# Kernel tuning notes

Hardware: AMD Instinct MI355X
Metric: run time of the kernel (lower is better)

Reference implementation:

```python
import jax, jax.numpy as jnp
import numpy as np
from jax import lax

DIM = 128; D_STATE = 16; D_CONV = 4; D_INNER = 256; DT_RANK = 8
N_HEADS = 4; SPARSE_RATIO = 0.5; LN_EPS = 1e-5


def rmsnorm(x, w):
    return x * lax.rsqrt(jnp.mean(x * x, axis=-1, keepdims=True) + 1e-5) * w


def layernorm(x, w, b):
    mu = jnp.mean(x, axis=-1, keepdims=True)
    var = jnp.mean((x - mu) ** 2, axis=-1, keepdims=True)
    return (x - mu) * lax.rsqrt(var + LN_EPS) * w + b


def mamba(x, in_proj_w, conv1d_w, conv1d_b, x_proj_w, dt_proj_w, dt_proj_b, A_log, Dp, out_proj_w):
    # x: (N, L, d_model) -> selective scan over L
    N, L, _ = x.shape
    xz = x @ in_proj_w.T                              # (N, L, 2*d_inner)
    xc, zg = jnp.split(xz, 2, axis=-1)
    xc = xc.transpose(0, 2, 1)                        # (N, d_inner, L)
    xc = lax.conv_general_dilated(xc, conv1d_w, (1,), [(D_CONV - 1, 0)],
                                  feature_group_count=D_INNER,
                                  dimension_numbers=('NCH', 'OIH', 'NCH'))
    xc = jax.nn.silu(xc + conv1d_b[None, :, None]).transpose(0, 2, 1)  # (N, L, d_inner)
    x_dbl = xc @ x_proj_w.T
    dt, Bm, Cm = jnp.split(x_dbl, [DT_RANK, DT_RANK + D_STATE], axis=-1)
    dt = jax.nn.softplus(dt @ dt_proj_w.T + dt_proj_b)  # (N, L, d_inner)
    A = -jnp.exp(A_log)                                  # (d_inner, d_state)

    def step(h, ts):
        dt_t, B_t, C_t, u_t = ts                         # (N,di),(N,ds),(N,ds),(N,di)
        h = h * jnp.exp(dt_t[:, :, None] * A) + (dt_t * u_t)[:, :, None] * B_t[:, None, :]
        y = jnp.einsum('nds,ns->nd', h, C_t)
        return h, y

    h0 = jnp.zeros((N, D_INNER, D_STATE), x.dtype)
    ts = (dt.transpose(1, 0, 2), Bm.transpose(1, 0, 2), Cm.transpose(1, 0, 2), xc.transpose(1, 0, 2))
    _, ys = lax.scan(step, h0, ts)
    y = ys.transpose(1, 0, 2) + xc * Dp
    y = y * jax.nn.silu(zg)
    return y @ out_proj_w.T


def setup_inputs() -> dict:
    key = jax.random.key(0)
    ks = jax.random.split(key, 16)
    s = 0.02
    B, T, C, H, W = 8, 8, 128, 32, 32
    rn = lambda k, shp: (jax.random.normal(k, shp, jnp.float32) * s)
    return {
        'x_in': jax.random.normal(ks[0], (B, T, C, H, W), jnp.float32),
        'norm1_w': jnp.ones((DIM,), jnp.float32),
        'in_proj_w': rn(ks[1], (2 * D_INNER, DIM)),
        'conv1d_w': rn(ks[2], (D_INNER, 1, D_CONV)),
        'conv1d_b': jnp.zeros((D_INNER,), jnp.float32),
        'x_proj_w': rn(ks[3], (DT_RANK + 2 * D_STATE, D_INNER)),
        'dt_proj_w': rn(ks[4], (D_INNER, DT_RANK)),
        'dt_proj_b': jax.random.uniform(ks[5], (D_INNER,), jnp.float32, -0.1, 0.1),
        'A_log': jnp.log(jnp.broadcast_to(jnp.arange(1, D_STATE + 1, dtype=jnp.float32), (D_INNER, D_STATE))),
        'D': jnp.ones((D_INNER,), jnp.float32),
        'out_proj_w': rn(ks[6], (DIM, D_INNER)),
        'r1_w': rn(ks[7], (DIM // 4, DIM, 3, 3)),
        'r1_b': jnp.zeros((DIM // 4,), jnp.float32),
        'r2_w': rn(ks[8], (1, DIM // 4, 1, 1)),
        'r2_b': jnp.zeros((1,), jnp.float32),
        'attn_in_w': rn(ks[9], (3 * DIM, DIM)),
        'attn_in_b': jnp.zeros((3 * DIM,), jnp.float32),
        'attn_out_w': rn(ks[10], (DIM, DIM)),
        'attn_out_b': jnp.zeros((DIM,), jnp.float32),
        'ln_w': jnp.ones((DIM,), jnp.float32),
        'ln_b': jnp.zeros((DIM,), jnp.float32),
        'current_epoch': 20,
    }


def reference(x_in, norm1_w, in_proj_w, conv1d_w, conv1d_b, x_proj_w, dt_proj_w, dt_proj_b,
              A_log, D, out_proj_w, r1_w, r1_b, r2_w, r2_b, attn_in_w, attn_in_b,
              attn_out_w, attn_out_b, ln_w, ln_b, current_epoch):
    B, T, C, H, W = x_in.shape
    N = H * W
    # annealed sparse ratio: current_epoch (static int) >= anneal_end -> target ratio
    ratio = SPARSE_RATIO if current_epoch >= 10 else (0.0 if current_epoch < 5 else SPARSE_RATIO * (current_epoch - 5) / 5.0)
    K = max(1, int(N * (1.0 - ratio)))
    # ---- learnable router scores (eval mode: no noise) ----
    xm = jnp.mean(x_in, axis=1)                       # (B,C,H,W)
    h1 = lax.conv_general_dilated(xm, r1_w, (1, 1), [(1, 1), (1, 1)],
                                  dimension_numbers=('NCHW', 'OIHW', 'NCHW')) + r1_b[None, :, None, None]
    h1 = jnp.where(h1 >= 0, h1, 0.01 * h1)            # LeakyReLU(0.01)
    sc = lax.conv_general_dilated(h1, r2_w, (1, 1), [(0, 0), (0, 0)],
                                  dimension_numbers=('NCHW', 'OIHW', 'NCHW')) + r2_b[None, :, None, None]
    scores = jax.nn.sigmoid(sc).reshape(B, N)
    _, idx = lax.top_k(scores, K)
    idx = jnp.sort(idx, axis=1)                        # (B,K)
    bi = jnp.arange(B)[:, None]
    x_flat = x_in.transpose(0, 3, 4, 1, 2).reshape(B, N, T, C)
    x_g = x_flat[bi, idx]                              # (B,K,T,C)
    s_g = scores[bi, idx]
    x_sp = x_g * (s_g / (lax.stop_gradient(s_g) + 1e-6))[:, :, None, None]  # STE scaling
    # ---- time mixing: Mamba on each kept spatial token ----
    z = rmsnorm(x_sp.reshape(B * K, T, C), norm1_w)
    z = mamba(z, in_proj_w, conv1d_w, conv1d_b, x_proj_w, dt_proj_w, dt_proj_b, A_log, D, out_proj_w)
    # ---- spatial self-attention over K tokens per time step ----
    zs = z.reshape(B, K, T, C).transpose(0, 2, 1, 3).reshape(B * T, K, C)
    qkv = zs @ attn_in_w.T + attn_in_b
    q, k, v = jnp.split(qkv, 3, axis=-1)
    dh = C // N_HEADS
    heads = lambda t: t.reshape(B * T, K, N_HEADS, dh).transpose(0, 2, 1, 3)
    q, k, v = heads(q), heads(k), heads(v)
    attn = jax.nn.softmax(jnp.einsum('bhqd,bhkd->bhqk', q, k) / np.sqrt(dh).astype(np.float32), axis=-1)
    o = jnp.einsum('bhqk,bhkd->bhqd', attn, v).transpose(0, 2, 1, 3).reshape(B * T, K, C)
    o = o @ attn_out_w.T + attn_out_b
    z_out = layernorm(zs + o, ln_w, ln_b)
    # ---- densify (scatter back) & residual ----
    upd = z_out.reshape(B, T, K, C).transpose(0, 2, 1, 3)  # (B,K,T,C)
    dense = jnp.zeros((B, N, T, C), x_in.dtype).at[bi, idx].set(upd)
    return x_in + dense.reshape(B, H, W, T, C).transpose(0, 3, 4, 1, 2)
```

## Files before the change

### kernel.cpp

```cpp
#include <hip/hip_runtime.h>
#include <hip/hip_bf16.h>

typedef __hip_bfloat16 bf16;
typedef __attribute__((ext_vector_type(8))) short short8;
typedef __attribute__((ext_vector_type(4))) float f32x4;

#define KK 512

__device__ float g_xm[1048576];
__device__ float g_h1[262144];
__device__ float g_scal[4096];
__device__ int   g_idx[4096];
__device__ float g_xg[4194304];
__device__ float g_zs[4194304];
__device__ float g_qkv[12582912];
__device__ float g_o[4194304];
__device__ float g_xz[16777216];
__device__ float g_xc[8388608];
__device__ float g_xdbl[1310720];
__device__ float g_y[8388608];
__device__ float g_wint[65536];
__device__ float g_wot[16384];
__device__ ushort g_wqkvh[49152];
__device__ ushort g_wouth[32768];
__device__ float g_A[4096];
__device__ float g_zo[4194304];

__device__ __forceinline__ float b2f(bf16 v) { return __bfloat162float(v); }

__device__ __forceinline__ ushort f2bu(float f) {
    union { float f; unsigned u; } v; v.f = f;
    unsigned r = v.u + 0x7fffu + ((v.u >> 16) & 1u);
    return (ushort)(r >> 16);
}

union U8 { short8 v; ushort u[8]; };

__global__ void k_mean(const float* __restrict__ x) {
    int id = blockIdx.x * 256 + threadIdx.x;
    int n = id & 1023;
    int c = (id >> 10) & 127;
    int b = id >> 17;
    float s = 0.f;
#pragma unroll
    for (int t = 0; t < 8; ++t)
        s += x[(((b * 8 + t) * 128 + c) << 10) + n];
    g_xm[id] = s * 0.125f;
}

__global__ __launch_bounds__(1024) void k_rconv1(const float* __restrict__ w) {
    __shared__ float xs[4][1024];
    int blk = blockIdx.x;
    int icc = blk & 31, b = blk >> 5;
    int ic0 = icc * 4;
    int tid = threadIdx.x;
    int x = tid & 31, y = tid >> 5;
#pragma unroll
    for (int i = 0; i < 4; ++i)
        xs[i][tid] = g_xm[b * 131072 + (ic0 + i) * 1024 + tid];
    __syncthreads();

    float xv[4][9];
#pragma unroll
    for (int i = 0; i < 4; ++i)
#pragma unroll
        for (int ky = 0; ky < 3; ++ky)
#pragma unroll
            for (int kx = 0; kx < 3; ++kx) {
                int yy = y + ky - 1, xx = x + kx - 1;
                bool ok = (yy >= 0) && (yy < 32) && (xx >= 0) && (xx < 32);
                xv[i][ky * 3 + kx] = ok ? xs[i][yy * 32 + xx] : 0.f;
            }

    float* rp = g_xz;
#pragma unroll 2
    for (int oc = 0; oc < 32; ++oc) {
        const float* wr = w + (oc * 128 + ic0) * 9;
        float acc = 0.f;
#pragma unroll
        for (int i = 0; i < 4; ++i)
#pragma unroll
            for (int t = 0; t < 9; ++t)
                acc += xv[i][t] * wr[i * 9 + t];
        rp[((size_t)(icc * 8 + b) * 32 + oc) * 1024 + tid] = acc;
    }
}

__global__ void k_rconv2(const float* __restrict__ bias) {
    int id = blockIdx.x * 256 + threadIdx.x;
    int oc = (id >> 10) & 31;
    const float* rp = g_xz;
    float acc = bias[oc];
#pragma unroll 8
    for (int icc = 0; icc < 32; ++icc)
        acc += rp[(size_t)icc * 262144 + id];
    g_h1[id] = acc >= 0.f ? acc : 0.01f * acc;
}

__global__ __launch_bounds__(1024) void k_topk(const float* __restrict__ r2w,
                                               const float* __restrict__ r2b) {
    __shared__ float sc[1024];
    __shared__ int flg[1024];
    int b = blockIdx.x;
    int n = threadIdx.x;
    float a = r2b[0];
#pragma unroll
    for (int ic = 0; ic < 32; ++ic)
        a += g_h1[b * 32768 + ic * 1024 + n] * r2w[ic];
    float s = 1.f / (1.f + expf(-a));
    sc[n] = s;
    __syncthreads();
    int rank = 0;
    for (int j = 0; j < 1024; ++j) {
        float v = sc[j];
        rank += (v > s) || (v == s && j < n);
    }
    int sel = rank < KK ? 1 : 0;
    flg[n] = sel;
    __syncthreads();
    for (int d = 1; d < 1024; d <<= 1) {
        int add = (n >= d) ? flg[n - d] : 0;
        __syncthreads();
        flg[n] += add;
        __syncthreads();
    }
    if (sel) {
        int pos = (flg[n] - 1) & 511;
        g_idx[b * KK + pos] = n;
        g_scal[b * KK + pos] = s / (s + 1e-6f);
    }
}

__global__ __launch_bounds__(256) void k_gather(const float* __restrict__ x) {
    __shared__ float lds[16][1024];
    int blk = blockIdx.x;
    int cchunk = blk & 7;
    int t = (blk >> 3) & 7;
    int b = blk >> 6;
    int c0 = cchunk * 16;
    int tid = threadIdx.x;
    const float* src = x + ((size_t)(b * 8 + t) * 128 + c0) * 1024;
#pragma unroll
    for (int r = 0; r < 64; ++r) {
        int e = tid + r * 256;
        lds[e >> 10][e & 1023] = src[e];
    }
    __syncthreads();
#pragma unroll
    for (int half = 0; half < 2; ++half) {
        int k = tid + half * 256;
        int n = g_idx[b * KK + k] & 1023;
        float scl = fminf(fmaxf(g_scal[b * KK + k], 0.f), 1.f);
        float* dst = g_xg + ((size_t)(b * 512 + k) * 8 + t) * 128 + c0;
#pragma unroll
        for (int cc = 0; cc < 16; ++cc)
            dst[cc] = lds[cc][n] * scl;
    }
}

__global__ void k_wt(const float* __restrict__ w_in, const float* __restrict__ w_out,
                     const float* __restrict__ w_ao, const float* __restrict__ A_log,
                     const float* __restrict__ w_qkv) {
    int e = blockIdx.x * 256 + threadIdx.x;
    if (e < 65536) { int j = e >> 7; int c = e & 127; g_wint[c * 512 + j] = w_in[e]; }
    if (e < 32768) { g_wouth[e] = f2bu(w_out[e]); }
    if (e < 16384) { int i = e >> 7; int c = e & 127; g_wot[c * 128 + i] = w_ao[e]; }
    if (e < 49152) { g_wqkvh[e] = f2bu(w_qkv[e]); }
    if (e < 4096)  { g_A[e] = -expf(A_log[e]);
                     g_scal[e] = 1.0f; g_idx[e] = e & 511; }
}

template<int KTOT, int NTOT, int JW, int NSPLIT, int MODE>
__global__ __launch_bounds__(512) void k_proj(const float* __restrict__ bias,
                                              const float* __restrict__ conv_w,
                                              const float* __restrict__ conv_b) {
    __shared__ float Xs[64 * 129];
    const float* A  = (MODE == 0) ? g_xg : g_o;
    const float* Bt = (MODE == 0) ? g_wint : g_wot;
    float* Cc       = g_xz;
    int blk = blockIdx.x;
    int ncol0 = (blk % NSPLIT) * (NTOT / NSPLIT);
    int row0 = (blk / NSPLIT) * 64;
    int tid = threadIdx.x;
    int lane = tid & 63;
    int j0 = __builtin_amdgcn_readfirstlane(ncol0 + (tid >> 6) * JW);
    float acc[JW];
#pragma unroll
    for (int j = 0; j < JW; ++j) acc[j] = 0.f;
    float ss = 0.f;

    for (int kc = 0; kc < KTOT; kc += 128) {
        __syncthreads();
#pragma unroll
        for (int i = 0; i < 4; ++i) {
            int e4 = tid + i * 512;
            int r = e4 >> 5, c4 = e4 & 31;
            float4 v = *(const float4*)&A[(size_t)(row0 + r) * KTOT + kc + c4 * 4];
            float* xp = &Xs[r * 129 + c4 * 4];
            xp[0] = v.x; xp[1] = v.y; xp[2] = v.z; xp[3] = v.w;
        }
        __syncthreads();
        const float* xr = &Xs[lane * 129];
        const float* wbase = Bt + (size_t)kc * NTOT + j0;
#pragma unroll 2
        for (int k4 = 0; k4 < 32; ++k4) {
            float a0 = xr[k4 * 4 + 0], a1 = xr[k4 * 4 + 1];
            float a2 = xr[k4 * 4 + 2], a3 = xr[k4 * 4 + 3];
            if (MODE == 0) {
                float4 nw = *(const float4*)(bias + kc + k4 * 4);
                ss += a0 * a0 + a1 * a1 + a2 * a2 + a3 * a3;
                a0 *= nw.x; a1 *= nw.y; a2 *= nw.z; a3 *= nw.w;
            }
            const float* wb = wbase + (size_t)k4 * 4 * NTOT;
#pragma unroll
            for (int jj = 0; jj < JW / 4; ++jj) {
                float4 w0 = *(const float4*)(wb + jj * 4);
                float4 w1 = *(const float4*)(wb + NTOT + jj * 4);
                float4 w2 = *(const float4*)(wb + 2 * NTOT + jj * 4);
                float4 w3 = *(const float4*)(wb + 3 * NTOT + jj * 4);
                float s0 = acc[jj*4+0], s1 = acc[jj*4+1], s2 = acc[jj*4+2], s3 = acc[jj*4+3];
                s0 += a0 * w0.x; s1 += a0 * w0.y; s2 += a0 * w0.z; s3 += a0 * w0.w;
                s0 += a1 * w1.x; s1 += a1 * w1.y; s2 += a1 * w1.z; s3 += a1 * w1.w;
                s0 += a2 * w2.x; s1 += a2 * w2.y; s2 += a2 * w2.z; s3 += a2 * w2.w;
                s0 += a3 * w3.x; s1 += a3 * w3.y; s2 += a3 * w3.z; s3 += a3 * w3.w;
                acc[jj*4+0] = s0; acc[jj*4+1] = s1; acc[jj*4+2] = s2; acc[jj*4+3] = s3;
            }
        }
    }

    if (MODE == 0) {
        float rstd = rsqrtf(ss * (1.f / 128.f) + 1e-5f);
#pragma unroll
        for (int j = 0; j < JW; ++j) acc[j] *= rstd;
    }

    int row = row0 + lane;
    if (MODE == 0 && j0 < 256) {
        int t = lane & 7;
        float* dst = g_xc + (size_t)row * 256 + j0;
#pragma unroll
        for (int jj = 0; jj < JW / 4; ++jj) {
            float4 vv;
            float* vp = (float*)&vv;
#pragma unroll
            for (int q = 0; q < 4; ++q) {
                int j = jj * 4 + q;
                float x3 = acc[j];
                float x2 = __shfl_up(x3, 1, 64); if (t < 1) x2 = 0.f;
                float x1 = __shfl_up(x3, 2, 64); if (t < 2) x1 = 0.f;
                float x0 = __shfl_up(x3, 3, 64); if (t < 3) x0 = 0.f;
                float4 w4 = *(const float4*)(conv_w + (j0 + j) * 4);
                float v = x0 * w4.x + x1 * w4.y + x2 * w4.z + x3 * w4.w + conv_b[j0 + j];
                vp[q] = v * __builtin_amdgcn_rcpf(1.f + __expf(-v));
            }
            *(float4*)(dst + jj * 4) = vv;
        }
    } else if (MODE == 3) {
        __shared__ float red1[8][64];
        __shared__ float red2[8][64];
        int w = tid >> 6;
        __syncthreads();
#pragma unroll
        for (int i = 0; i < 4; ++i) {
            int e4 = tid + i * 512;
            int r = e4 >> 5, c4 = e4 & 31;
            float4 v = *(const float4*)&g_zs[(size_t)(row0 + r) * 128 + c4 * 4];
            float* xp = &Xs[r * 129 + c4 * 4];
            xp[0] = v.x; xp[1] = v.y; xp[2] = v.z; xp[3] = v.w;
        }
        __syncthreads();
        float s1 = 0.f, s2 = 0.f;
#pragma unroll
        for (int j = 0; j < JW; ++j) {
            acc[j] += bias[j0 + j] + Xs[lane * 129 + j0 + j];
            s1 += acc[j]; s2 += acc[j] * acc[j];
        }
        red1[w][lane] = s1; red2[w][lane] = s2;
        __syncthreads();
        float S1 = 0.f, S2 = 0.f;
#pragma unroll
        for (int ww = 0; ww < 8; ++ww) { S1 += red1[ww][lane]; S2 += red2[ww][lane]; }
        float mu = S1 * (1.f / 128.f);
        float var = S2 * (1.f / 128.f) - mu * mu;
        float rstd2 = rsqrtf(fmaxf(var, 0.f) + 1e-5f);
        int bt = row >> 9, ktok = row & 511;
        float* zb = g_zo + (size_t)(bt * 128 + j0) * 512 + ktok;
#pragma unroll
        for (int j = 0; j < JW; ++j)
            zb[(size_t)j * 512] = (acc[j] - mu) * rstd2 * conv_w[j0 + j] + conv_b[j0 + j];
    } else {
        float* dst = Cc + (size_t)row * NTOT + j0;
#pragma unroll
        for (int jj = 0; jj < JW / 4; ++jj)
            *(float4*)(dst + jj * 4) =
                make_float4(acc[jj*4], acc[jj*4+1], acc[jj*4+2], acc[jj*4+3]);
    }
}

__global__ __launch_bounds__(256) void k_outm() {
    __shared__ ushort As[8][64][40];
    __shared__ ushort Bs[128][40];
    int row0 = blockIdx.x * 64;
    int tid = threadIdx.x;
    int w = tid >> 6, lane = tid & 63;
    int c = lane & 15, g = lane >> 4;

    {
        int r = tid >> 2, ksb = tid & 3;
#pragma unroll
        for (int kb2 = 0; kb2 < 2; ++kb2) {
            int kb = ksb + kb2 * 4;
            const float* src = g_y + (size_t)(row0 + r) * 256 + kb * 32;
#pragma unroll
            for (int i = 0; i < 4; ++i) {
                float4 a = *(const float4*)(src + i * 8);
                float4 b = *(const float4*)(src + i * 8 + 4);
                U8 t;
                t.u[0] = f2bu(a.x); t.u[1] = f2bu(a.y); t.u[2] = f2bu(a.z); t.u[3] = f2bu(a.w);
                t.u[4] = f2bu(b.x); t.u[5] = f2bu(b.y); t.u[6] = f2bu(b.z); t.u[7] = f2bu(b.w);
                *(short8*)&As[kb][r][i * 8] = t.v;
            }
        }
    }

    f32x4 acc[8];
    f32x4 zero = {0.f, 0.f, 0.f, 0.f};
#pragma unroll
    for (int nt = 0; nt < 8; ++nt) acc[nt] = zero;

    for (int ks = 0; ks < 8; ++ks) {
        __syncthreads();
#pragma unroll
        for (int i = 0; i < 2; ++i) {
            int e = tid + i * 256;
            int n = e >> 2, q = e & 3;
            *(short8*)&Bs[n][q * 8] =
                *(const short8*)&g_wouth[n * 256 + ks * 32 + q * 8];
        }
        __syncthreads();
        short8 af = *(const short8*)&As[ks][w * 16 + c][g * 8];
#pragma unroll
        for (int nt = 0; nt < 8; ++nt) {
            short8 bf8 = *(const short8*)&Bs[nt * 16 + c][g * 8];
            acc[nt] = __builtin_amdgcn_mfma_f32_16x16x32_bf16(af, bf8, acc[nt], 0, 0, 0);
        }
    }

#pragma unroll
    for (int r = 0; r < 4; ++r) {
        int row = row0 + w * 16 + g * 4 + r;
        int bb = row >> 12, kk2 = (row >> 3) & 511, t = row & 7;
        float* dst = g_zs + ((size_t)((bb * 8 + t) * 512 + kk2)) * 128 + c;
#pragma unroll
        for (int nt = 0; nt < 8; ++nt)
            dst[nt * 16] = acc[nt][r];
    }
}

__global__ __launch_bounds__(256) void k_qkvm(const float* __restrict__ bias) {
    __shared__ ushort As[4][64][40];
    __shared__ ushort Bs[384][40];
    int row0 = blockIdx.x * 64;
    int tid = threadIdx.x;
    int w = tid >> 6, lane = tid & 63;
    int c = lane & 15, g = lane >> 4;

    {
        int r = tid >> 2, ksb = tid & 3;
        const float* src = g_zs + (size_t)(row0 + r) * 128 + ksb * 32;
#pragma unroll
        for (int i = 0; i < 4; ++i) {
            float4 a = *(const float4*)(src + i * 8);
            float4 b = *(const float4*)(src + i * 8 + 4);
            U8 t;
            t.u[0] = f2bu(a.x); t.u[1] = f2bu(a.y); t.u[2] = f2bu(a.z); t.u[3] = f2bu(a.w);
            t.u[4] = f2bu(b.x); t.u[5] = f2bu(b.y); t.u[6] = f2bu(b.z); t.u[7] = f2bu(b.w);
            *(short8*)&As[ksb][r][i * 8] = t.v;
        }
    }

    f32x4 acc[24];
    f32x4 zero = {0.f, 0.f, 0.f, 0.f};
#pragma unroll
    for (int nt = 0; nt < 24; ++nt) acc[nt] = zero;

    for (int ks = 0; ks < 4; ++ks) {
        __syncthreads();
#pragma unroll
        for (int i = 0; i < 6; ++i) {
            int e = tid + i * 256;
            int n = e >> 2, q = e & 3;
            *(short8*)&Bs[n][q * 8] =
                *(const short8*)&g_wqkvh[n * 128 + ks * 32 + q * 8];
        }
        __syncthreads();
        short8 af = *(const short8*)&As[ks][w * 16 + c][g * 8];
#pragma unroll
        for (int nt = 0; nt < 24; ++nt) {
            short8 bf8 = *(const short8*)&Bs[nt * 16 + c][g * 8];
            acc[nt] = __builtin_amdgcn_mfma_f32_16x16x32_bf16(af, bf8, acc[nt], 0, 0, 0);
        }
    }

#pragma unroll
    for (int nt = 0; nt < 24; ++nt) {
        float bv = bias[nt * 16 + c];
#pragma unroll
        for (int r = 0; r < 4; ++r) {
            int tok = row0 + w * 16 + g * 4 + r;
            g_qkv[(size_t)tok * 384 + nt * 16 + c] = acc[nt][r] + bv;
        }
    }
}

__global__ __launch_bounds__(512, 2) void k_xproj(const float* __restrict__ w_xp) {
    __shared__ float Xs[64][66];
    int row0 = blockIdx.x * 64;
    int tid = threadIdx.x;
    int lane = tid & 63;
    int j0 = __builtin_amdgcn_readfirstlane((tid >> 6) * 5);
    float acc0 = 0.f, acc1 = 0.f, acc2 = 0.f, acc3 = 0.f, acc4 = 0.f;

    for (int kc = 0; kc < 4; ++kc) {
        __syncthreads();
#pragma unroll
        for (int i = 0; i < 2; ++i) {
            int e = tid + i * 512;
            int r = e >> 4, k4 = e & 15;
            *(float4*)&Xs[r][k4 * 4] =
                *(const float4*)&g_xc[(size_t)(row0 + r) * 256 + kc * 64 + k4 * 4];
        }
        __syncthreads();
#pragma unroll
        for (int k4 = 0; k4 < 16; ++k4) {
            float4 x4 = *(const float4*)&Xs[lane][k4 * 4];
            const float* wb = w_xp + kc * 64 + k4 * 4;
            float4 w0 = *(const float4*)(wb + (j0 + 0) * 256);
            float4 w1 = *(const float4*)(wb + (j0 + 1) * 256);
            float4 w2 = *(const float4*)(wb + (j0 + 2) * 256);
            float4 w3 = *(const float4*)(wb + (j0 + 3) * 256);
            float4 w4 = *(const float4*)(wb + (j0 + 4) * 256);
            acc0 += x4.x * w0.x + x4.y * w0.y + x4.z * w0.z + x4.w * w0.w;
            acc1 += x4.x * w1.x + x4.y * w1.y + x4.z * w1.z + x4.w * w1.w;
            acc2 += x4.x * w2.x + x4.y * w2.y + x4.z * w2.z + x4.w * w2.w;
            acc3 += x4.x * w3.x + x4.y * w3.y + x4.z * w3.z + x4.w * w3.w;
            acc4 += x4.x * w4.x + x4.y * w4.y + x4.z * w4.z + x4.w * w4.w;
        }
    }
    float* dst = g_xdbl + (size_t)(row0 + lane) * 40 + j0;
    dst[0] = acc0; dst[1] = acc1; dst[2] = acc2; dst[3] = acc3; dst[4] = acc4;
}

__global__ __launch_bounds__(256, 2) void k_scan2(const float* __restrict__ w_dt,
                        const float* __restrict__ b_dt, const float* __restrict__ Dp) {
    int tok = blockIdx.x;
    int d = threadIdx.x;
    const float* xzr = g_xz + (size_t)tok * 4096;
    const float* xcr = g_xc + (size_t)tok * 2048;
    const float* xd0 = g_xdbl + (size_t)tok * 320;
    float* yr = g_y + (size_t)tok * 2048;

    float4 wdt0 = *(const float4*)(w_dt + d * 8);
    float4 wdt1 = *(const float4*)(w_dt + d * 8 + 4);
    float bdt = b_dt[d];
    float Dd = Dp[d];
    float Av[16], h[16];
#pragma unroll
    for (int s = 0; s < 4; ++s) {
        float4 a4 = *(const float4*)(g_A + d * 16 + s * 4);
        Av[4*s] = a4.x; Av[4*s+1] = a4.y; Av[4*s+2] = a4.z; Av[4*s+3] = a4.w;
    }
#pragma unroll
    for (int s = 0; s < 16; ++s) h[s] = 0.f;

#pragma unroll
    for (int t = 0; t < 8; ++t) {
        const float* xd = xd0 + t * 40;
        float dtv = bdt
            + xd[0] * wdt0.x + xd[1] * wdt0.y + xd[2] * wdt0.z + xd[3] * wdt0.w
            + xd[4] * wdt1.x + xd[5] * wdt1.y + xd[6] * wdt1.z + xd[7] * wdt1.w;
        dtv = dtv > 20.f ? dtv : logf(1.f + expf(dtv));
        float u = xcr[t * 256 + d];
        float db = dtv * u;
        float y = 0.f;
#pragma unroll
        for (int s = 0; s < 16; ++s) {
            h[s] = h[s] * __expf(dtv * Av[s]) + db * xd[8 + s];
            y += h[s] * xd[24 + s];
        }
        y += u * Dd;
        float zg = xzr[t * 512 + 256 + d];
        y *= zg * __builtin_amdgcn_rcpf(1.f + __expf(-zg));
        yr[t * 256 + d] = y;
    }
}

#define ATTN_LDS 74240
__global__ __launch_bounds__(256, 2) void k_attn3() {
    extern __shared__ char smem[];
    ushort* Kl = (ushort*)smem;
    ushort* Vt = (ushort*)(smem + 40960);
    ushort* Pl = (ushort*)smem;
    __shared__ float statsM[4][32];
    __shared__ float statsS[4][32];

    int blk = blockIdx.x;
    int qt = blk & 3, h = (blk >> 2) & 3, bt = blk >> 4;
    int q0 = qt * 32;
    int tid = threadIdx.x;
    int w = tid >> 6, lane = tid & 63;
    int c = lane & 15, g = lane >> 4;
    const float* QKV = g_qkv + (size_t)bt * 512 * 384;
    const float rs = 0.17677669529663687f;

    short8 qf[2];
#pragma unroll
    for (int i = 0; i < 2; ++i) {
        const float* qp = QKV + (size_t)(q0 + i * 16 + c) * 384 + h * 32 + g * 8;
        float4 a = *(const float4*)qp;
        float4 b = *(const float4*)(qp + 4);
        U8 t;
        t.u[0] = f2bu(a.x * rs); t.u[1] = f2bu(a.y * rs);
        t.u[2] = f2bu(a.z * rs); t.u[3] = f2bu(a.w * rs);
        t.u[4] = f2bu(b.x * rs); t.u[5] = f2bu(b.y * rs);
        t.u[6] = f2bu(b.z * rs); t.u[7] = f2bu(b.w * rs);
        qf[i] = t.v;
    }

#pragma unroll
    for (int r = 0; r < 8; ++r) {
        int tok = r * 64 + (tid >> 2);
        int dblk = (tid & 3) * 8;
        const float* kp = QKV + (size_t)tok * 384 + 128 + h * 32 + dblk;
        float4 ka = *(const float4*)kp,       kb4 = *(const float4*)(kp + 4);
        float4 va = *(const float4*)(kp+128), vb4 = *(const float4*)(kp + 132);
        U8 t;
        t.u[0] = f2bu(ka.x); t.u[1] = f2bu(ka.y); t.u[2] = f2bu(ka.z); t.u[3] = f2bu(ka.w);
        t.u[4] = f2bu(kb4.x); t.u[5] = f2bu(kb4.y); t.u[6] = f2bu(kb4.z); t.u[7] = f2bu(kb4.w);
        *(short8*)&Kl[tok * 40 + dblk] = t.v;
        Vt[(dblk + 0) * 520 + tok] = f2bu(va.x);
        Vt[(dblk + 1) * 520 + tok] = f2bu(va.y);
        Vt[(dblk + 2) * 520 + tok] = f2bu(va.z);
        Vt[(dblk + 3) * 520 + tok] = f2bu(va.w);
        Vt[(dblk + 4) * 520 + tok] = f2bu(vb4.x);
        Vt[(dblk + 5) * 520 + tok] = f2bu(vb4.y);
        Vt[(dblk + 6) * 520 + tok] = f2bu(vb4.z);
        Vt[(dblk + 7) * 520 + tok] = f2bu(vb4.w);
    }
    __syncthreads();

    int kbase = w * 128;
    f32x4 S[2][8];
    f32x4 zero = {0.f, 0.f, 0.f, 0.f};
#pragma unroll
    for (int ks = 0; ks < 8; ++ks) {
        short8 kf = *(const short8*)&Kl[(kbase + ks * 16 + c) * 40 + g * 8];
        S[0][ks] = __builtin_amdgcn_mfma_f32_16x16x32_bf16(qf[0], kf, zero, 0, 0, 0);
        S[1][ks] = __builtin_amdgcn_mfma_f32_16x16x32_bf16(qf[1], kf, zero, 0, 0, 0);
    }

    float pmax[2][4];
#pragma unroll
    for (int i = 0; i < 2; ++i)
#pragma unroll
        for (int r = 0; r < 4; ++r) {
            float m = S[i][0][r];
#pragma unroll
            for (int ks = 1; ks < 8; ++ks) m = fmaxf(m, S[i][ks][r]);
            pmax[i][r] = m;
        }
#pragma unroll
    for (int msk = 1; msk <= 8; msk <<= 1)
#pragma unroll
        for (int i = 0; i < 2; ++i)
#pragma unroll
            for (int r = 0; r < 4; ++r)
                pmax[i][r] = fmaxf(pmax[i][r], __shfl_xor(pmax[i][r], msk, 64));
    if (c == 0) {
#pragma unroll
        for (int i = 0; i < 2; ++i)
#pragma unroll
            for (int r = 0; r < 4; ++r)
                statsM[w][i * 16 + g * 4 + r] = pmax[i][r];
    }
    __syncthreads();

    float psum[2][4];
#pragma unroll
    for (int i = 0; i < 2; ++i)
#pragma unroll
        for (int r = 0; r < 4; ++r) {
            int q = i * 16 + g * 4 + r;
            float m = fmaxf(fmaxf(statsM[0][q], statsM[1][q]),
                            fmaxf(statsM[2][q], statsM[3][q]));
            float ps = 0.f;
#pragma unroll
            for (int ks = 0; ks < 8; ++ks) {
                float p = __expf(S[i][ks][r] - m);
                ps += p;
                Pl[q * 520 + kbase + ks * 16 + c] = f2bu(p);
            }
            psum[i][r] = ps;
        }
#pragma unroll
    for (int msk = 1; msk <= 8; msk <<= 1)
#pragma unroll
        for (int i = 0; i < 2; ++i)
#pragma unroll
            for (int r = 0; r < 4; ++r)
                psum[i][r] += __shfl_xor(psum[i][r], msk, 64);
    if (c == 0) {
#pragma unroll
        for (int i = 0; i < 2; ++i)
#pragma unroll
            for (int r = 0; r < 4; ++r)
                statsS[w][i * 16 + g * 4 + r] = psum[i][r];
    }
    __syncthreads();

    f32x4 o[2][2];
    o[0][0] = zero; o[0][1] = zero; o[1][0] = zero; o[1][1] = zero;
#pragma unroll
    for (int kst = 0; kst < 4; ++kst) {
        int k0 = kbase + kst * 32;
        short8 pa0 = *(const short8*)&Pl[(c) * 520 + k0 + g * 8];
        short8 pa1 = *(const short8*)&Pl[(16 + c) * 520 + k0 + g * 8];
        short8 vb0 = *(const short8*)&Vt[(c) * 520 + k0 + g * 8];
        short8 vb1 = *(const short8*)&Vt[(16 + c) * 520 + k0 + g * 8];
        o[0][0] = __builtin_amdgcn_mfma_f32_16x16x32_bf16(pa0, vb0, o[0][0], 0, 0, 0);
        o[0][1] = __builtin_amdgcn_mfma_f32_16x16x32_bf16(pa0, vb1, o[0][1], 0, 0, 0);
        o[1][0] = __builtin_amdgcn_mfma_f32_16x16x32_bf16(pa1, vb0, o[1][0], 0, 0, 0);
        o[1][1] = __builtin_amdgcn_mfma_f32_16x16x32_bf16(pa1, vb1, o[1][1], 0, 0, 0);
    }
    __syncthreads();

    float* Op = (float*)smem;
#pragma unroll
    for (int i = 0; i < 2; ++i)
#pragma unroll
        for (int jd = 0; jd < 2; ++jd)
#pragma unroll
            for (int r = 0; r < 4; ++r)
                Op[(w * 32 + i * 16 + g * 4 + r) * 33 + jd * 16 + c] = o[i][jd][r];
    __syncthreads();

    int q = tid >> 3;
    int d0 = (tid & 7) * 4;
    float lrow = statsS[0][q] + statsS[1][q] + statsS[2][q] + statsS[3][q];
    float inv = 1.f / lrow;
    float* orow = g_o + ((size_t)(bt * 512) + q0 + q) * 128 + h * 32 + d0;
#pragma unroll
    for (int dd = 0; dd < 4; ++dd) {
        float s = Op[(0 * 32 + q) * 33 + d0 + dd] + Op[(1 * 32 + q) * 33 + d0 + dd]
                + Op[(2 * 32 + q) * 33 + d0 + dd] + Op[(3 * 32 + q) * 33 + d0 + dd];
        orow[dd] = s * inv;
    }
}

__global__ __launch_bounds__(256) void k_fin2(const float* __restrict__ x_in,
                                              float* __restrict__ out) {
    __shared__ float dense[1024];
    int R = blockIdx.x;
    int bt = R >> 7;
    int b = bt >> 3;
    int tid = threadIdx.x;
#pragma unroll
    for (int i = 0; i < 4; ++i) dense[tid + i * 256] = 0.f;
    __syncthreads();
#pragma unroll
    for (int hh = 0; hh < 2; ++hh) {
        int k = tid + hh * 256;
        int n = g_idx[b * KK + k] & 1023;
        dense[n] = g_zo[(size_t)R * 512 + k];
    }
    __syncthreads();
    const float4* xr = (const float4*)(x_in + (size_t)R * 1024);
    const float4* dn = (const float4*)dense;
    float4* orr = (float4*)(out + (size_t)R * 1024);
    float4 xv = xr[tid], dv = dn[tid];
    float4 ov;
    ov.x = xv.x + dv.x; ov.y = xv.y + dv.y; ov.z = xv.z + dv.z; ov.w = xv.w + dv.w;
    orr[tid] = ov;
}

extern "C" void kernel_launch(void* const* d_in, const int* in_sizes, int n_in,
                              void* d_out, int out_size, void* d_ws, size_t ws_size,
                              hipStream_t stream) {
    const float* x_in      = (const float*)d_in[0];
    const float* norm1_w   = (const float*)d_in[1];
    const float* in_proj_w = (const float*)d_in[2];
    const float* conv1d_w  = (const float*)d_in[3];
    const float* conv1d_b  = (const float*)d_in[4];
    const float* x_proj_w  = (const float*)d_in[5];
    const float* dt_proj_w = (const float*)d_in[6];
    const float* dt_proj_b = (const float*)d_in[7];
    const float* A_log     = (const float*)d_in[8];
    const float* Dp        = (const float*)d_in[9];
    const float* out_proj_w= (const float*)d_in[10];
    const float* r1_w      = (const float*)d_in[11];
    const float* r1_b      = (const float*)d_in[12];
    const float* r2_w      = (const float*)d_in[13];
    const float* r2_b      = (const float*)d_in[14];
    const float* attn_in_w = (const float*)d_in[15];
    const float* attn_in_b = (const float*)d_in[16];
    const float* attn_out_w= (const float*)d_in[17];
    const float* attn_out_b= (const float*)d_in[18];
    const float* ln_w      = (const float*)d_in[19];
    const float* ln_b      = (const float*)d_in[20];

    float* out = (float*)d_out;

    static bool attr_set = false;
    if (!attr_set) {
        hipFuncSetAttribute(reinterpret_cast<const void*>(k_attn3),
                            hipFuncAttributeMaxDynamicSharedMemorySize, ATTN_LDS);
        attr_set = true;
    }

    k_wt<<<256, 256, 0, stream>>>(in_proj_w, out_proj_w, attn_out_w, A_log, attn_in_w);
    k_mean<<<4096, 256, 0, stream>>>(x_in);
    k_rconv1<<<256, 1024, 0, stream>>>(r1_w);
    k_rconv2<<<1024, 256, 0, stream>>>(r1_b);
    k_topk<<<8, 1024, 0, stream>>>(r2_w, r2_b);
    k_gather<<<512, 256, 0, stream>>>(x_in);
    k_proj<128, 512, 32, 2, 0><<<1024, 512, 0, stream>>>(norm1_w, conv1d_w, conv1d_b);
    k_xproj<<<512, 512, 0, stream>>>(x_proj_w);
    k_scan2<<<4096, 256, 0, stream>>>(dt_proj_w, dt_proj_b, Dp);
    k_outm<<<512, 256, 0, stream>>>();
    k_qkvm<<<512, 256, 0, stream>>>(attn_in_b);
    k_attn3<<<1024, 256, ATTN_LDS, stream>>>();
    k_proj<128, 128, 16, 1, 3><<<512, 512, 0, stream>>>(attn_out_b, ln_w, ln_b);
    k_fin2<<<8192, 256, 0, stream>>>(x_in, out);
}
```

Baseline: 470.1 us.

## Use split-bf16 MFMA for in-projection and split depthwise conv into own kernel

The fp32 FMA in-projection GEMM is replaced by a matrix-core kernel that splits activations and weights into high and low bf16 parts and runs three MFMAs per tile, keeping near-fp32 accuracy. RMSNorm weights are folded into the preprocessed weights, and the row scale is applied after the matmul. The causal conv plus SiLU, previously fused into the GEMM epilogue, now runs as a separate kernel that reads g_xz, which adds a global round trip and an extra launch. The out-proj/LayerNorm path is moved unchanged into a dedicated kernel.

```diff
diff --git a/kernel.cpp b/kernel.cpp
--- a/kernel.cpp
+++ b/kernel.cpp
@@ -19,7 +19,8 @@
 __device__ float g_xc[8388608];
 __device__ float g_xdbl[1310720];
 __device__ float g_y[8388608];
-__device__ float g_wint[65536];
+__device__ ushort g_winth[65536];
+__device__ ushort g_wintl[65536];
 __device__ float g_wot[16384];
 __device__ ushort g_wqkvh[49152];
 __device__ ushort g_wouth[32768];
@@ -32,6 +33,9 @@
     union { float f; unsigned u; } v; v.f = f;
     unsigned r = v.u + 0x7fffu + ((v.u >> 16) & 1u);
     return (ushort)(r >> 16);
+}
+__device__ __forceinline__ float bu2f(ushort u) {
+    union { unsigned u; float f; } v; v.u = ((unsigned)u) << 16; return v.f;
 }
 
 union U8 { short8 v; ushort u[8]; };
@@ -160,9 +164,15 @@
 
 __global__ void k_wt(const float* __restrict__ w_in, const float* __restrict__ w_out,
                      const float* __restrict__ w_ao, const float* __restrict__ A_log,
-                     const float* __restrict__ w_qkv) {
+                     const float* __restrict__ w_qkv, const float* __restrict__ nw) {
     int e = blockIdx.x * 256 + threadIdx.x;
-    if (e < 65536) { int j = e >> 7; int c = e & 127; g_wint[c * 512 + j] = w_in[e]; }
+    if (e < 65536) {
+        int k = e & 127;
+        float wf = w_in[e] * nw[k];
+        ushort h = f2bu(wf);
+        g_winth[e] = h;
+        g_wintl[e] = f2bu(wf - bu2f(h));
+    }
     if (e < 32768) { g_wouth[e] = f2bu(w_out[e]); }
     if (e < 16384) { int i = e >> 7; int c = e & 127; g_wot[c * 128 + i] = w_ao[e]; }
     if (e < 49152) { g_wqkvh[e] = f2bu(w_qkv[e]); }
@@ -170,130 +180,101 @@
                      g_scal[e] = 1.0f; g_idx[e] = e & 511; }
 }
 
-template<int KTOT, int NTOT, int JW, int NSPLIT, int MODE>
-__global__ __launch_bounds__(512) void k_proj(const float* __restrict__ bias,
-                                              const float* __restrict__ conv_w,
+__global__ __launch_bounds__(256) void k_inm() {
+    __shared__ ushort Ah[4][64][40];
+    __shared__ ushort Al[4][64][40];
+    __shared__ ushort Bh[128][40];
+    __shared__ ushort Bl[128][40];
+    __shared__ float sR[64];
+    int blk = blockIdx.x;
+    int ncol0 = (blk & 3) * 128;
+    int row0 = (blk >> 2) * 64;
+    int tid = threadIdx.x;
+    int w = tid >> 6, lane = tid & 63;
+    int c = lane & 15, g = lane >> 4;
+
+    {
+        int r = tid >> 2, ksb = tid & 3;
+        const float* src = g_xg + (size_t)(row0 + r) * 128 + ksb * 32;
+        float ss = 0.f;
+#pragma unroll
+        for (int i = 0; i < 4; ++i) {
+            float4 a = *(const float4*)(src + i * 8);
+            float4 b = *(const float4*)(src + i * 8 + 4);
+            float xv[8] = {a.x, a.y, a.z, a.w, b.x, b.y, b.z, b.w};
+            U8 th, tl;
+#pragma unroll
+            for (int q = 0; q < 8; ++q) {
+                float x = xv[q];
+                ss += x * x;
+                ushort h = f2bu(x);
+                th.u[q] = h;
+                tl.u[q] = f2bu(x - bu2f(h));
+            }
+            *(short8*)&Ah[ksb][r][i * 8] = th.v;
+            *(short8*)&Al[ksb][r][i * 8] = tl.v;
+        }
+        ss += __shfl_xor(ss, 1, 64);
+        ss += __shfl_xor(ss, 2, 64);
+        if ((tid & 3) == 0) sR[r] = rsqrtf(ss * (1.f / 128.f) + 1e-5f);
+    }
+
+    f32x4 acc[8];
+    f32x4 zero = {0.f, 0.f, 0.f, 0.f};
+#pragma unroll
+    for (int nt = 0; nt < 8; ++nt) acc[nt] = zero;
+
+    for (int ks = 0; ks < 4; ++ks) {
+        __syncthreads();
+#pragma unroll
+        for (int i = 0; i < 2; ++i) {
+            int e = tid + i * 256;
+            int n = e >> 2, q = e & 3;
+            *(short8*)&Bh[n][q * 8] =
+                *(const short8*)&g_winth[(ncol0 + n) * 128 + ks * 32 + q * 8];
+            *(short8*)&Bl[n][q * 8] =
+                *(const short8*)&g_wintl[(ncol0 + n) * 128 + ks * 32 + q * 8];
+        }
+        __syncthreads();
+        short8 ah = *(const short8*)&Ah[ks][w * 16 + c][g * 8];
+        short8 al = *(const short8*)&Al[ks][w * 16 + c][g * 8];
+#pragma unroll
+        for (int nt = 0; nt < 8; ++nt) {
+            short8 bh = *(const short8*)&Bh[nt * 16 + c][g * 8];
+            short8 bl = *(const short8*)&Bl[nt * 16 + c][g * 8];
+            acc[nt] = __builtin_amdgcn_mfma_f32_16x16x32_bf16(ah, bh, acc[nt], 0, 0, 0);
+            acc[nt] = __builtin_amdgcn_mfma_f32_16x16x32_bf16(ah, bl, acc[nt], 0, 0, 0);
+            acc[nt] = __builtin_amdgcn_mfma_f32_16x16x32_bf16(al, bh, acc[nt], 0, 0, 0);
+        }
+    }
+
+#pragma unroll
+    for (int r = 0; r < 4; ++r) {
+        int rowl = w * 16 + g * 4 + r;
+        float rs_ = sR[rowl];
+        float* dst = g_xz + (size_t)(row0 + rowl) * 512 + ncol0 + c;
+#pragma unroll
+        for (int nt = 0; nt < 8; ++nt)
+            dst[nt * 16] = acc[nt][r] * rs_;
+    }
+}
+
+__global__ __launch_bounds__(256) void k_conv(const float* __restrict__ conv_w,
                                               const float* __restrict__ conv_b) {
-    __shared__ float Xs[64 * 129];
-    const float* A  = (MODE == 0) ? g_xg : g_o;
-    const float* Bt = (MODE == 0) ? g_wint : g_wot;
-    float* Cc       = g_xz;
-    int blk = blockIdx.x;
-    int ncol0 = (blk % NSPLIT) * (NTOT / NSPLIT);
-    int row0 = (blk / NSPLIT) * 64;
-    int tid = threadIdx.x;
-    int lane = tid & 63;
-    int j0 = __builtin_amdgcn_readfirstlane(ncol0 + (tid >> 6) * JW);
-    float acc[JW];
-#pragma unroll
-    for (int j = 0; j < JW; ++j) acc[j] = 0.f;
-    float ss = 0.f;
-
-    for (int kc = 0; kc < KTOT; kc += 128) {
-        __syncthreads();
-#pragma unroll
-        for (int i = 0; i < 4; ++i) {
-            int e4 = tid + i * 512;
-            int r = e4 >> 5, c4 = e4 & 31;
-            float4 v = *(const float4*)&A[(size_t)(row0 + r) * KTOT + kc + c4 * 4];
-            float* xp = &Xs[r * 129 + c4 * 4];
-            xp[0] = v.x; xp[1] = v.y; xp[2] = v.z; xp[3] = v.w;
-        }
-        __syncthreads();
-        const float* xr = &Xs[lane * 129];
-        const float* wbase = Bt + (size_t)kc * NTOT + j0;
-#pragma unroll 2
-        for (int k4 = 0; k4 < 32; ++k4) {
-            float a0 = xr[k4 * 4 + 0], a1 = xr[k4 * 4 + 1];
-            float a2 = xr[k4 * 4 + 2], a3 = xr[k4 * 4 + 3];
-            if (MODE == 0) {
-                float4 nw = *(const float4*)(bias + kc + k4 * 4);
-                ss += a0 * a0 + a1 * a1 + a2 * a2 + a3 * a3;
-                a0 *= nw.x; a1 *= nw.y; a2 *= nw.z; a3 *= nw.w;
-            }
-            const float* wb = wbase + (size_t)k4 * 4 * NTOT;
-#pragma unroll
-            for (int jj = 0; jj < JW / 4; ++jj) {
-                float4 w0 = *(const float4*)(wb + jj * 4);
-                float4 w1 = *(const float4*)(wb + NTOT + jj * 4);
-                float4 w2 = *(const float4*)(wb + 2 * NTOT + jj * 4);
-                float4 w3 = *(const float4*)(wb + 3 * NTOT + jj * 4);
-                float s0 = acc[jj*4+0], s1 = acc[jj*4+1], s2 = acc[jj*4+2], s3 = acc[jj*4+3];
-                s0 += a0 * w0.x; s1 += a0 * w0.y; s2 += a0 * w0.z; s3 += a0 * w0.w;
-                s0 += a1 * w1.x; s1 += a1 * w1.y; s2 += a1 * w1.z; s3 += a1 * w1.w;
-                s0 += a2 * w2.x; s1 += a2 * w2.y; s2 += a2 * w2.z; s3 += a2 * w2.w;
-                s0 += a3 * w3.x; s1 += a3 * w3.y; s2 += a3 * w3.z; s3 += a3 * w3.w;
-                acc[jj*4+0] = s0; acc[jj*4+1] = s1; acc[jj*4+2] = s2; acc[jj*4+3] = s3;
-            }
-        }
-    }
-
-    if (MODE == 0) {
-        float rstd = rsqrtf(ss * (1.f / 128.f) + 1e-5f);
-#pragma unroll
-        for (int j = 0; j < JW; ++j) acc[j] *= rstd;
-    }
-
-    int row = row0 + lane;
-    if (MODE == 0 && j0 < 256) {
-        int t = lane & 7;
-        float* dst = g_xc + (size_t)row * 256 + j0;
-#pragma unroll
-        for (int jj = 0; jj < JW / 4; ++jj) {
-            float4 vv;
-            float* vp = (float*)&vv;
-#pragma unroll
-            for (int q = 0; q < 4; ++q) {
-                int j = jj * 4 + q;
-                float x3 = acc[j];
-                float x2 = __shfl_up(x3, 1, 64); if (t < 1) x2 = 0.f;
-                float x1 = __shfl_up(x3, 2, 64); if (t < 2) x1 = 0.f;
-                float x0 = __shfl_up(x3, 3, 64); if (t < 3) x0 = 0.f;
-                float4 w4 = *(const float4*)(conv_w + (j0 + j) * 4);
-                float v = x0 * w4.x + x1 * w4.y + x2 * w4.z + x3 * w4.w + conv_b[j0 + j];
-                vp[q] = v * __builtin_amdgcn_rcpf(1.f + __expf(-v));
-            }
-            *(float4*)(dst + jj * 4) = vv;
-        }
-    } else if (MODE == 3) {
-        __shared__ float red1[8][64];
-        __shared__ float red2[8][64];
-        int w = tid >> 6;
-        __syncthreads();
-#pragma unroll
-        for (int i = 0; i < 4; ++i) {
-            int e4 = tid + i * 512;
-            int r = e4 >> 5, c4 = e4 & 31;
-            float4 v = *(const float4*)&g_zs[(size_t)(row0 + r) * 128 + c4 * 4];
-            float* xp = &Xs[r * 129 + c4 * 4];
-            xp[0] = v.x; xp[1] = v.y; xp[2] = v.z; xp[3] = v.w;
-        }
-        __syncthreads();
-        float s1 = 0.f, s2 = 0.f;
-#pragma unroll
-        for (int j = 0; j < JW; ++j) {
-            acc[j] += bias[j0 + j] + Xs[lane * 129 + j0 + j];
-            s1 += acc[j]; s2 += acc[j] * acc[j];
-        }
-        red1[w][lane] = s1; red2[w][lane] = s2;
-        __syncthreads();
-        float S1 = 0.f, S2 = 0.f;
-#pragma unroll
-        for (int ww = 0; ww < 8; ++ww) { S1 += red1[ww][lane]; S2 += red2[ww][lane]; }
-        float mu = S1 * (1.f / 128.f);
-        float var = S2 * (1.f / 128.f) - mu * mu;
-        float rstd2 = rsqrtf(fmaxf(var, 0.f) + 1e-5f);
-        int bt = row >> 9, ktok = row & 511;
-        float* zb = g_zo + (size_t)(bt * 128 + j0) * 512 + ktok;
-#pragma unroll
-        for (int j = 0; j < JW; ++j)
-            zb[(size_t)j * 512] = (acc[j] - mu) * rstd2 * conv_w[j0 + j] + conv_b[j0 + j];
-    } else {
-        float* dst = Cc + (size_t)row * NTOT + j0;
-#pragma unroll
-        for (int jj = 0; jj < JW / 4; ++jj)
-            *(float4*)(dst + jj * 4) =
-                make_float4(acc[jj*4], acc[jj*4+1], acc[jj*4+2], acc[jj*4+3]);
+    int tok = blockIdx.x;
+    int d = threadIdx.x;
+    const float* xzr = g_xz + (size_t)tok * 4096;
+    float* xcr = g_xc + (size_t)tok * 2048;
+    float4 w4 = *(const float4*)(conv_w + d * 4);
+    float cb = conv_b[d];
+    float x0 = 0.f, x1 = 0.f, x2 = 0.f;
+#pragma unroll
+    for (int t = 0; t < 8; ++t) {
+        float x3 = xzr[t * 512 + d];
+        float v = x0 * w4.x + x1 * w4.y + x2 * w4.z + x3 * w4.w + cb;
+        v = v * __builtin_amdgcn_rcpf(1.f + __expf(-v));
+        xcr[t * 256 + d] = v;
+        x0 = x1; x1 = x2; x2 = x3;
     }
 }
 
@@ -655,6 +636,85 @@
                 + Op[(2 * 32 + q) * 33 + d0 + dd] + Op[(3 * 32 + q) * 33 + d0 + dd];
         orow[dd] = s * inv;
     }
+}
+
+__global__ __launch_bounds__(512) void k_fino(const float* __restrict__ bias,
+                                              const float* __restrict__ ln_w,
+                                              const float* __restrict__ ln_b) {
+    __shared__ float Xs[64 * 129];
+    __shared__ float red1[8][64];
+    __shared__ float red2[8][64];
+    int row0 = blockIdx.x * 64;
+    int tid = threadIdx.x;
+    int lane = tid & 63;
+    int w = tid >> 6;
+    int j0 = __builtin_amdgcn_readfirstlane(w * 16);
+    float acc[16];
+#pragma unroll
+    for (int j = 0; j < 16; ++j) acc[j] = 0.f;
+
+    {
+#pragma unroll
+        for (int i = 0; i < 4; ++i) {
+            int e4 = tid + i * 512;
+            int r = e4 >> 5, c4 = e4 & 31;
+            float4 v = *(const float4*)&g_o[(size_t)(row0 + r) * 128 + c4 * 4];
+            float* xp = &Xs[r * 129 + c4 * 4];
+            xp[0] = v.x; xp[1] = v.y; xp[2] = v.z; xp[3] = v.w;
+        }
+        __syncthreads();
+        const float* xr = &Xs[lane * 129];
+#pragma unroll 2
+        for (int k4 = 0; k4 < 32; ++k4) {
+            float a0 = xr[k4 * 4 + 0], a1 = xr[k4 * 4 + 1];
+            float a2 = xr[k4 * 4 + 2], a3 = xr[k4 * 4 + 3];
+            const float* wb = g_wot + (size_t)k4 * 4 * 128 + j0;
+#pragma unroll
+            for (int jj = 0; jj < 4; ++jj) {
+                float4 w0 = *(const float4*)(wb + jj * 4);
+                float4 w1 = *(const float4*)(wb + 128 + jj * 4);
+                float4 w2 = *(const float4*)(wb + 256 + jj * 4);
+                float4 w3 = *(const float4*)(wb + 384 + jj * 4);
+                float s0 = acc[jj*4+0], s1 = acc[jj*4+1], s2 = acc[jj*4+2], s3 = acc[jj*4+3];
+                s0 += a0 * w0.x; s1 += a0 * w0.y; s2 += a0 * w0.z; s3 += a0 * w0.w;
+                s0 += a1 * w1.x; s1 += a1 * w1.y; s2 += a1 * w1.z; s3 += a1 * w1.w;
+                s0 += a2 * w2.x; s1 += a2 * w2.y; s2 += a2 * w2.z; s3 += a2 * w2.w;
+                s0 += a3 * w3.x; s1 += a3 * w3.y; s2 += a3 * w3.z; s3 += a3 * w3.w;
+                acc[jj*4+0] = s0; acc[jj*4+1] = s1; acc[jj*4+2] = s2; acc[jj*4+3] = s3;
+            }
+        }
+    }
+
+    __syncthreads();
+#pragma unroll
+    for (int i = 0; i < 4; ++i) {
+        int e4 = tid + i * 512;
+        int r = e4 >> 5, c4 = e4 & 31;
+        float4 v = *(const float4*)&g_zs[(size_t)(row0 + r) * 128 + c4 * 4];
+        float* xp = &Xs[r * 129 + c4 * 4];
+        xp[0] = v.x; xp[1] = v.y; xp[2] = v.z; xp[3] = v.w;
+    }
+    __syncthreads();
+    float s1 = 0.f, s2 = 0.f;
+#pragma unroll
+    for (int j = 0; j < 16; ++j) {
+        acc[j] += bias[j0 + j] + Xs[lane * 129 + j0 + j];
+        s1 += acc[j]; s2 += acc[j] * acc[j];
+    }
+    red1[w][lane] = s1; red2[w][lane] = s2;
+    __syncthreads();
+    float S1 = 0.f, S2 = 0.f;
+#pragma unroll
+    for (int ww = 0; ww < 8; ++ww) { S1 += red1[ww][lane]; S2 += red2[ww][lane]; }
+    float mu = S1 * (1.f / 128.f);
+    float var = S2 * (1.f / 128.f) - mu * mu;
+    float rstd2 = rsqrtf(fmaxf(var, 0.f) + 1e-5f);
+    int row = row0 + lane;
+    int bt = row >> 9, ktok = row & 511;
+    float* zb = g_zo + (size_t)(bt * 128 + j0) * 512 + ktok;
+#pragma unroll
+    for (int j = 0; j < 16; ++j)
+        zb[(size_t)j * 512] = (acc[j] - mu) * rstd2 * ln_w[j0 + j] + ln_b[j0 + j];
 }
 
 __global__ __launch_bounds__(256) void k_fin2(const float* __restrict__ x_in,
@@ -717,18 +777,20 @@
         attr_set = true;
     }
 
-    k_wt<<<256, 256, 0, stream>>>(in_proj_w, out_proj_w, attn_out_w, A_log, attn_in_w);
+    k_wt<<<256, 256, 0, stream>>>(in_proj_w, out_proj_w, attn_out_w, A_log,
+                                  attn_in_w, norm1_w);
     k_mean<<<4096, 256, 0, stream>>>(x_in);
     k_rconv1<<<256, 1024, 0, stream>>>(r1_w);
     k_rconv2<<<1024, 256, 0, stream>>>(r1_b);
     k_topk<<<8, 1024, 0, stream>>>(r2_w, r2_b);
     k_gather<<<512, 256, 0, stream>>>(x_in);
-    k_proj<128, 512, 32, 2, 0><<<1024, 512, 0, stream>>>(norm1_w, conv1d_w, conv1d_b);
+    k_inm<<<2048, 256, 0, stream>>>();
+    k_conv<<<4096, 256, 0, stream>>>(conv1d_w, conv1d_b);
     k_xproj<<<512, 512, 0, stream>>>(x_proj_w);
     k_scan2<<<4096, 256, 0, stream>>>(dt_proj_w, dt_proj_b, Dp);
     k_outm<<<512, 256, 0, stream>>>();
     k_qkvm<<<512, 256, 0, stream>>>(attn_in_b);
     k_attn3<<<1024, 256, ATTN_LDS, stream>>>();
-    k_proj<128, 128, 16, 1, 3><<<512, 512, 0, stream>>>(attn_out_b, ln_w, ln_b);
+    k_fino<<<512, 512, 0, stream>>>(attn_out_b, ln_w, ln_b);
     k_fin2<<<8192, 256, 0, stream>>>(x_in, out);
 }
```

Measured after the change: 452.7 us. 1.04x faster.
